# Optimization experiments

Hardware: AMD Instinct MI355X
Metric: run time of the kernel (lower is better)

Reference implementation:

```python
import jax, jax.numpy as jnp
import numpy as np

N = 4096
F_IN = 512
F_OUT = 64
H = 8
ALPHA = 0.2
NEG_BIG = -9e15


def setup_inputs() -> dict:
    key = jax.random.key(0)
    ks = jax.random.split(key, 7)
    h = jax.random.normal(ks[0], (N, F_IN), dtype=jnp.float32)
    mask = jax.random.randint(ks[1], (N, N), 0, 2, dtype=jnp.int32)
    # per-head linear W: weight [H, F_IN, F_OUT], bias [H, F_OUT] (xavier-ish scale)
    w_scale = 1.414 * np.sqrt(6.0 / (F_IN + F_OUT))
    W = jax.random.uniform(ks[2], (H, F_IN, F_OUT), dtype=jnp.float32, minval=-w_scale, maxval=w_scale)
    bW = jnp.zeros((H, F_OUT), dtype=jnp.float32)
    # attention linear A: [2*F_OUT, 1] split into a_l (acts on Wh_i) and a_r (acts on Wh_j)
    a_scale = 1.414 * np.sqrt(6.0 / (2 * F_OUT + 1))
    a_l = jax.random.uniform(ks[3], (H, F_OUT), dtype=jnp.float32, minval=-a_scale, maxval=a_scale)
    a_r = jax.random.uniform(ks[4], (H, F_OUT), dtype=jnp.float32, minval=-a_scale, maxval=a_scale)
    bA = jnp.zeros((H,), dtype=jnp.float32)
    return {"h": h, "mask": mask, "W": W, "bW": bW, "a_l": a_l, "a_r": a_r, "bA": bA}


def reference(h, mask, W, bW, a_l, a_r, bA):
    # Wh: [H, N, F_OUT]
    Wh = jnp.einsum('ni,hio->hno', h, W) + bW[:, None, :]
    # A([Wh_i ; Wh_j]) decomposed as outer sum: e[h,i,j] = a_l.Wh_i + a_r.Wh_j + bA
    el = jnp.einsum('hno,ho->hn', Wh, a_l)  # [H, N]
    er = jnp.einsum('hno,ho->hn', Wh, a_r)  # [H, N]
    e = el[:, :, None] + er[:, None, :] + bA[:, None, None]  # [H, N, N]
    e = jax.nn.leaky_relu(e, negative_slope=ALPHA)
    e = jnp.where(mask[None] > 0, e, NEG_BIG)
    a = jax.nn.softmax(e, axis=-1)  # softmax over neighbors j (dim=1 in torch)
    # dropout omitted (eval mode / deterministic reference)
    aWh = jnp.einsum('hij,hjo->hio', a, Wh)  # [H, N, F_OUT]
    out = jax.nn.elu(aWh)  # last=False
    # concat heads along feature dim -> [N, H*F_OUT]
    return jnp.transpose(out, (1, 0, 2)).reshape(N, H * F_OUT)
```

## Files before the change

### kernel.cpp

```cpp
#include <hip/hip_runtime.h>
#include <hip/hip_bf16.h>

#define NN 4096
#define FIN 512
#define FOUT 64
#define NH 8
#define ALPHA 0.2f

typedef unsigned int uint;
typedef unsigned short ushort;
typedef unsigned char uchar;
typedef unsigned long long ull;
typedef __attribute__((ext_vector_type(8))) short short8;
typedef __attribute__((ext_vector_type(4))) float floatx4;

__device__ __forceinline__ float bf2f(ushort s) { return __uint_as_float(((uint)s) << 16); }
__device__ __forceinline__ ushort f2bf(float f) {
    uint u = __float_as_uint(f);
    u += 0x7fffu + ((u >> 16) & 1u);
    return (ushort)(u >> 16);
}

__device__ __forceinline__ int detect_bf16(const ushort* __restrict__ hraw) {
    int lane = threadIdx.x & 63;
    float a = fabsf(bf2f(hraw[2 * lane]));
    ull bal = __ballot(a >= 1e-3f && a <= 100.0f);
    return __popcll(bal) >= 32;
}

#define PM_BLKS 8192
#define CV_BLKS 1024
#define TW_BLKS 32

__global__ __launch_bounds__(256) void prep_kernel(
    const int* __restrict__ mask, uchar* __restrict__ mb,
    const void* __restrict__ hraw, ushort* __restrict__ bh,
    const void* __restrict__ Wraw, ushort* __restrict__ WT)
{
    const int b = blockIdx.x, t = threadIdx.x;
    if (b < PM_BLKS) {
        size_t gid = (size_t)b * 256 + t;
        const int* p = mask + gid * 8;
        int4 aa = *(const int4*)p;
        int4 bb = *(const int4*)(p + 4);
        uint by = (uint)(aa.x > 0)        | ((uint)(aa.y > 0) << 1)
                | ((uint)(aa.z > 0) << 2) | ((uint)(aa.w > 0) << 3)
                | ((uint)(bb.x > 0) << 4) | ((uint)(bb.y > 0) << 5)
                | ((uint)(bb.z > 0) << 6) | ((uint)(bb.w > 0) << 7);
        mb[gid] = (uchar)by;
    } else if (b < PM_BLKS + CV_BLKS) {
        int isbf = detect_bf16((const ushort*)hraw);
        size_t e0 = ((size_t)(b - PM_BLKS) * 256 + t) * 8;
        if (isbf) {
            *(uint4*)(bh + e0) = *(const uint4*)((const ushort*)hraw + e0);
        } else {
            const float* s = (const float*)hraw + e0;
            float4 f0 = *(const float4*)s;
            float4 f1 = *(const float4*)(s + 4);
            uint4 o;
            o.x = (uint)f2bf(f0.x) | ((uint)f2bf(f0.y) << 16);
            o.y = (uint)f2bf(f0.z) | ((uint)f2bf(f0.w) << 16);
            o.z = (uint)f2bf(f1.x) | ((uint)f2bf(f1.y) << 16);
            o.w = (uint)f2bf(f1.z) | ((uint)f2bf(f1.w) << 16);
            *(uint4*)(bh + e0) = o;
        }
    } else {
        int isbf = detect_bf16((const ushort*)hraw);
        int b2 = b - PM_BLKS - CV_BLKS;
        int h = b2 >> 2, kq = b2 & 3;
        int o = t & 63, sub = t >> 6;
        int kbase = kq * 128 + sub * 32;
        uint pk[16];
#pragma unroll
        for (int kk = 0; kk < 32; kk += 2) {
            float v0, v1;
            size_t s0 = ((size_t)h * FIN + kbase + kk) * FOUT + o;
            size_t s1 = s0 + FOUT;
            if (isbf) { v0 = bf2f(((const ushort*)Wraw)[s0]); v1 = bf2f(((const ushort*)Wraw)[s1]); }
            else      { v0 = ((const float*)Wraw)[s0];        v1 = ((const float*)Wraw)[s1]; }
            pk[kk >> 1] = (uint)f2bf(v0) | ((uint)f2bf(v1) << 16);
        }
        ushort* dst = WT + ((size_t)h * FOUT + o) * FIN + kbase;
#pragma unroll
        for (int q = 0; q < 4; q++)
            *(uint4*)(dst + q * 8) = make_uint4(pk[q*4], pk[q*4+1], pk[q*4+2], pk[q*4+3]);
    }
}

__global__ __launch_bounds__(256) void khv_kernel(const float* __restrict__ er,
                                                  float* __restrict__ Kh,
                                                  float* __restrict__ vt,
                                                  float* __restrict__ zt) {
    __shared__ float red[256];
    int h = blockIdx.x >> 3, sl = blockIdx.x & 7, t = threadIdx.x;
    float m = -3.0e38f;
    for (int j = t; j < NN; j += 256) m = fmaxf(m, er[(size_t)h * NN + j]);
    red[t] = m;
    __syncthreads();
    for (int s = 128; s >= 1; s >>= 1) {
        if (t < s) red[t] = fmaxf(red[t], red[t + s]);
        __syncthreads();
    }
    float kh = red[0];
    if (t == 0 && sl == 0) Kh[h] = kh;
    int j = sl * 512 + t;
#pragma unroll
    for (int q = 0; q < 2; q++, j += 256) {
        float d = er[(size_t)h * NN + j] - kh;
        vt[(size_t)h * NN + j] = __expf(d);
        zt[(size_t)h * NN + j] = __expf(ALPHA * d);
    }
}

__global__ __launch_bounds__(256) void wh_kernel(
    const ushort* __restrict__ hmat, const ushort* __restrict__ WT,
    const void* __restrict__ bWr, const void* __restrict__ alr,
    const void* __restrict__ arr, const void* __restrict__ bAr,
    const ushort* __restrict__ hraw,
    ushort* __restrict__ WhT, float* __restrict__ el, float* __restrict__ er)
{
    __shared__ __align__(16) ushort sT[64][72];
    const int t = threadIdx.x, lane = t & 63, wid = t >> 6;
    const int head = blockIdx.y, rbase = blockIdx.x * 64;
    const int lm = lane & 15, lq = lane >> 4;

    floatx4 C[4];
#pragma unroll
    for (int cg = 0; cg < 4; cg++) C[cg] = (floatx4){0.f, 0.f, 0.f, 0.f};

    const ushort* Ap = hmat + (size_t)(rbase + wid * 16 + lm) * FIN + lq * 8;
    const ushort* Bp = WT + (size_t)head * FOUT * FIN + (size_t)lm * FIN + lq * 8;

#pragma unroll
    for (int kc = 0; kc < 16; kc++) {
        short8 a = *(const short8*)(Ap + kc * 32);
#pragma unroll
        for (int cg = 0; cg < 4; cg++) {
            short8 b = *(const short8*)(Bp + (size_t)cg * 16 * FIN + kc * 32);
            C[cg] = __builtin_amdgcn_mfma_f32_16x16x32_bf16(a, b, C[cg], 0, 0, 0);
        }
    }

    const int isbf = detect_bf16(hraw);
    float bA = isbf ? bf2f(((const ushort*)bAr)[head]) : ((const float*)bAr)[head];
    float pel[4] = {0.f, 0.f, 0.f, 0.f}, per[4] = {0.f, 0.f, 0.f, 0.f};
#pragma unroll
    for (int cg = 0; cg < 4; cg++) {
        int o = head * FOUT + cg * 16 + lm;
        float bw = isbf ? bf2f(((const ushort*)bWr)[o]) : ((const float*)bWr)[o];
        float av = isbf ? bf2f(((const ushort*)alr)[o]) : ((const float*)alr)[o];
        float rv = isbf ? bf2f(((const ushort*)arr)[o]) : ((const float*)arr)[o];
        ushort pk[4];
#pragma unroll
        for (int r = 0; r < 4; r++) {
            float v = C[cg][r] + bw;
            pel[r] += v * av;
            per[r] += v * rv;
            pk[r] = f2bf(v);
        }
        ushort4 p4; p4.x = pk[0]; p4.y = pk[1]; p4.z = pk[2]; p4.w = pk[3];
        *(ushort4*)(&sT[cg * 16 + lm][wid * 16 + lq * 4]) = p4;
    }
#pragma unroll
    for (int off = 1; off < 16; off <<= 1) {
#pragma unroll
        for (int r = 0; r < 4; r++) {
            pel[r] += __shfl_xor(pel[r], off);
            per[r] += __shfl_xor(per[r], off);
        }
    }
    if (lm == 0) {
#pragma unroll
        for (int r = 0; r < 4; r++) {
            int row = rbase + wid * 16 + lq * 4 + r;
            el[(size_t)head * NN + row] = pel[r];
            er[(size_t)head * NN + row] = per[r] + bA;
        }
    }
    __syncthreads();
    {
        int o = t >> 2, ch = t & 3;
        uint4 v0 = *(const uint4*)(&sT[o][ch * 16]);
        uint4 v1 = *(const uint4*)(&sT[o][ch * 16 + 8]);
        ushort* d = WhT + ((size_t)head * FOUT + o) * NN + rbase + ch * 16;
        *(uint4*)d = v0;
        *(uint4*)(d + 8) = v1;
    }
}

__device__ __forceinline__ uint ppair(float v0, float v1, float z0, float z1,
                                      uint m2, float ui, float wi) {
    float p0 = fmaxf(ui * v0, wi * z0);
    float p1 = fmaxf(ui * v1, wi * z1);
    uint k0 = (uint)0 - (m2 & 1u);
    uint k1 = (uint)0 - ((m2 >> 1) & 1u);
    p0 = __uint_as_float(__float_as_uint(p0) & k0);
    p1 = __uint_as_float(__float_as_uint(p1) & k1);
    __hip_bfloat162 r = __float22bfloat162_rn(make_float2(p0, p1));
    return *(uint*)&r;
}

__device__ __forceinline__ short8 pgen8(float4 va, float4 vb, float4 za, float4 zb,
                                        uint mby, float ui, float wi) {
    union { uint4 u; short8 s; } c;
    c.u.x = ppair(va.x, va.y, za.x, za.y, mby,      ui, wi);
    c.u.y = ppair(va.z, va.w, za.z, za.w, mby >> 2, ui, wi);
    c.u.z = ppair(vb.x, vb.y, zb.x, zb.y, mby >> 4, ui, wi);
    c.u.w = ppair(vb.z, vb.w, zb.z, zb.w, mby >> 6, ui, wi);
    return c.s;
}

#define VZLOAD(S, j0) do {                                      \
    v##S##a = *(const float4*)(gvt + (j0) + sh8);               \
    v##S##b = *(const float4*)(gvt + (j0) + sh8 + 4);           \
    v##S##c = *(const float4*)(gvt + (j0) + 32 + sh8);          \
    v##S##d = *(const float4*)(gvt + (j0) + 32 + sh8 + 4);      \
    z##S##a = *(const float4*)(gzt + (j0) + sh8);               \
    z##S##b = *(const float4*)(gzt + (j0) + sh8 + 4);           \
    z##S##c = *(const float4*)(gzt + (j0) + 32 + sh8);          \
    z##S##d = *(const float4*)(gzt + (j0) + 32 + sh8 + 4);      \
} while (0)

__global__ __launch_bounds__(128, 1) void attn_kernel(
    const uchar* __restrict__ mb,
    const ushort* __restrict__ WhT,
    const float* __restrict__ el, const float* __restrict__ Kh,
    const float* __restrict__ vt, const float* __restrict__ zt,
    const ushort* __restrict__ hraw,
    void* __restrict__ outv)
{
    __shared__ __align__(16) ushort sB[2][64 * 72];

    const int t = threadIdx.x, lane = t & 63, wid = t >> 6;
    const int b = blockIdx.x;
    const int head = b & 7;
    const int ibase = (b >> 3) * 64;
    const int lm = lane & 15, lq = lane >> 4;
    const int sh8 = lq * 8;

    const float kh = Kh[head];
    const int rowa = ibase + wid * 32 + lm;
    const float xa = el[(size_t)head * NN + rowa] + kh;
    const float xb = el[(size_t)head * NN + rowa + 16] + kh;
    const float Ma = fmaxf(xa, ALPHA * xa);
    const float Mb = fmaxf(xb, ALPHA * xb);
    const float uia = __expf(xa - Ma), wia = __expf(ALPHA * xa - Ma);
    const float uib = __expf(xb - Mb), wib = __expf(ALPHA * xb - Mb);

    const int so = t >> 1;
    const int sc = (t & 1) * 32;
    const ushort* gB = WhT + ((size_t)head * FOUT + so) * NN + sc;
    const float* gvt = vt + (size_t)head * NN;
    const float* gzt = zt + (size_t)head * NN;
    const uchar* mra = mb + (size_t)rowa * 512;
    const uchar* mrb = mra + 16 * 512;

    uint4 rr0, rr1, rr2, rr3;
    uint2 mka_s, mkb_s;

    auto gload = [&](int j0) {
        rr0 = *(const uint4*)(gB + j0);
        rr1 = *(const uint4*)(gB + j0 + 8);
        rr2 = *(const uint4*)(gB + j0 + 16);
        rr3 = *(const uint4*)(gB + j0 + 24);
        mka_s = *(const uint2*)(mra + (j0 >> 3));
        mkb_s = *(const uint2*)(mrb + (j0 >> 3));
    };
    auto lwrite = [&](int buf) {
        ushort* d = &sB[buf][so * 72 + sc];
        *(uint4*)(d)      = rr0;
        *(uint4*)(d + 8)  = rr1;
        *(uint4*)(d + 16) = rr2;
        *(uint4*)(d + 24) = rr3;
    };

    float4 v0a, v0b, v0c, v0d, z0a, z0b, z0c, z0d;
    float4 v1a, v1b, v1c, v1d, z1a, z1b, z1c, z1d;

    const short8 ones = {0x3F80, 0x3F80, 0x3F80, 0x3F80, 0x3F80, 0x3F80, 0x3F80, 0x3F80};
    floatx4 Z = {0.f, 0.f, 0.f, 0.f};
    floatx4 C0 = Z, C1 = Z, C2 = Z, C3 = Z, Cd0 = Z;
    floatx4 C4 = Z, C5 = Z, C6 = Z, C7 = Z, Cd1 = Z;

    auto compute = [&](int buf, uint2 mka, uint2 mkb,
                       float4 va, float4 vb, float4 vc, float4 vd,
                       float4 za, float4 zb, float4 zc, float4 zd) {
        uint m0a = (mka.x >> sh8) & 0xFFu;
        uint m1a = (mka.y >> sh8) & 0xFFu;
        uint m0b = (mkb.x >> sh8) & 0xFFu;
        uint m1b = (mkb.y >> sh8) & 0xFFu;
        short8 a0 = pgen8(va, vb, za, zb, m0a, uia, wia);
        short8 a1 = pgen8(vc, vd, zc, zd, m1a, uia, wia);
        short8 a2 = pgen8(va, vb, za, zb, m0b, uib, wib);
        short8 a3 = pgen8(vc, vd, zc, zd, m1b, uib, wib);
        const ushort* base = &sB[buf][0];
        short8 b00 = *(const short8*)(base + (0  + lm) * 72 + sh8);
        short8 b10 = *(const short8*)(base + (16 + lm) * 72 + sh8);
        short8 b20 = *(const short8*)(base + (32 + lm) * 72 + sh8);
        short8 b30 = *(const short8*)(base + (48 + lm) * 72 + sh8);
        Cd0 = __builtin_amdgcn_mfma_f32_16x16x32_bf16(a0, ones, Cd0, 0, 0, 0);
        Cd1 = __builtin_amdgcn_mfma_f32_16x16x32_bf16(a2, ones, Cd1, 0, 0, 0);
        C0 = __builtin_amdgcn_mfma_f32_16x16x32_bf16(a0, b00, C0, 0, 0, 0);
        C4 = __builtin_amdgcn_mfma_f32_16x16x32_bf16(a2, b00, C4, 0, 0, 0);
        C1 = __builtin_amdgcn_mfma_f32_16x16x32_bf16(a0, b10, C1, 0, 0, 0);
        C5 = __builtin_amdgcn_mfma_f32_16x16x32_bf16(a2, b10, C5, 0, 0, 0);
        C2 = __builtin_amdgcn_mfma_f32_16x16x32_bf16(a0, b20, C2, 0, 0, 0);
        C6 = __builtin_amdgcn_mfma_f32_16x16x32_bf16(a2, b20, C6, 0, 0, 0);
        C3 = __builtin_amdgcn_mfma_f32_16x16x32_bf16(a0, b30, C3, 0, 0, 0);
        C7 = __builtin_amdgcn_mfma_f32_16x16x32_bf16(a2, b30, C7, 0, 0, 0);
        short8 b01 = *(const short8*)(base + (0  + lm) * 72 + 32 + sh8);
        short8 b11 = *(const short8*)(base + (16 + lm) * 72 + 32 + sh8);
        short8 b21 = *(const short8*)(base + (32 + lm) * 72 + 32 + sh8);
        short8 b31 = *(const short8*)(base + (48 + lm) * 72 + 32 + sh8);
        Cd0 = __builtin_amdgcn_mfma_f32_16x16x32_bf16(a1, ones, Cd0, 0, 0, 0);
        Cd1 = __builtin_amdgcn_mfma_f32_16x16x32_bf16(a3, ones, Cd1, 0, 0, 0);
        C0 = __builtin_amdgcn_mfma_f32_16x16x32_bf16(a1, b01, C0, 0, 0, 0);
        C4 = __builtin_amdgcn_mfma_f32_16x16x32_bf16(a3, b01, C4, 0, 0, 0);
        C1 = __builtin_amdgcn_mfma_f32_16x16x32_bf16(a1, b11, C1, 0, 0, 0);
        C5 = __builtin_amdgcn_mfma_f32_16x16x32_bf16(a3, b11, C5, 0, 0, 0);
        C2 = __builtin_amdgcn_mfma_f32_16x16x32_bf16(a1, b21, C2, 0, 0, 0);
        C6 = __builtin_amdgcn_mfma_f32_16x16x32_bf16(a3, b21, C6, 0, 0, 0);
        C3 = __builtin_amdgcn_mfma_f32_16x16x32_bf16(a1, b31, C3, 0, 0, 0);
        C7 = __builtin_amdgcn_mfma_f32_16x16x32_bf16(a3, b31, C7, 0, 0, 0);
    };

    uint2 mka0, mkb0, mka1, mkb1;
    gload(0);
    lwrite(0);
    mka0 = mka_s; mkb0 = mkb_s;
    gload(64);
    VZLOAD(0, 0);
    __syncthreads();

    for (int it = 0; it < 64; it += 2) {
        lwrite(1);
        mka1 = mka_s; mkb1 = mkb_s;
        gload(((it + 2) & 63) * 64);
        VZLOAD(1, (it + 1) * 64);
        compute(0, mka0, mkb0, v0a, v0b, v0c, v0d, z0a, z0b, z0c, z0d);
        __syncthreads();
        lwrite(0);
        mka0 = mka_s; mkb0 = mkb_s;
        gload(((it + 3) & 63) * 64);
        VZLOAD(0, ((it + 2) & 63) * 64);
        compute(1, mka1, mkb1, v1a, v1b, v1c, v1d, z1a, z1b, z1c, z1d);
        __syncthreads();
    }

    const int isbf = detect_bf16(hraw);
#pragma unroll
    for (int r = 0; r < 4; r++) {
        int ra = ibase + wid * 32 + lq * 4 + r;
        int rb = ra + 16;
        float inva = 1.f / Cd0[r];
        float invb = 1.f / Cd1[r];
        float x0 = C0[r] * inva; x0 = (x0 > 0.f) ? x0 : __expf(x0) - 1.f;
        float x1 = C1[r] * inva; x1 = (x1 > 0.f) ? x1 : __expf(x1) - 1.f;
        float x2 = C2[r] * inva; x2 = (x2 > 0.f) ? x2 : __expf(x2) - 1.f;
        float x3 = C3[r] * inva; x3 = (x3 > 0.f) ? x3 : __expf(x3) - 1.f;
        float y0 = C4[r] * invb; y0 = (y0 > 0.f) ? y0 : __expf(y0) - 1.f;
        float y1 = C5[r] * invb; y1 = (y1 > 0.f) ? y1 : __expf(y1) - 1.f;
        float y2 = C6[r] * invb; y2 = (y2 > 0.f) ? y2 : __expf(y2) - 1.f;
        float y3 = C7[r] * invb; y3 = (y3 > 0.f) ? y3 : __expf(y3) - 1.f;
        size_t basea = (size_t)ra * (NH * FOUT) + head * FOUT + lm;
        size_t baseb = (size_t)rb * (NH * FOUT) + head * FOUT + lm;
        if (isbf) {
            ushort* o = (ushort*)outv;
            o[basea + 0]  = f2bf(x0);
            o[basea + 16] = f2bf(x1);
            o[basea + 32] = f2bf(x2);
            o[basea + 48] = f2bf(x3);
            o[baseb + 0]  = f2bf(y0);
            o[baseb + 16] = f2bf(y1);
            o[baseb + 32] = f2bf(y2);
            o[baseb + 48] = f2bf(y3);
        } else {
            float* o = (float*)outv;
            o[basea + 0]  = x0;
            o[basea + 16] = x1;
            o[basea + 32] = x2;
            o[basea + 48] = x3;
            o[baseb + 0]  = y0;
            o[baseb + 16] = y1;
            o[baseb + 32] = y2;
            o[baseb + 48] = y3;
        }
    }
}

extern "C" void kernel_launch(void* const* d_in, const int* in_sizes, int n_in,
                              void* d_out, int out_size, void* d_ws, size_t ws_size,
                              hipStream_t stream)
{
    const void* hraw = d_in[0];
    const int*  mask = (const int*)d_in[1];
    const void* Wraw = d_in[2];
    const void* bWr  = d_in[3];
    const void* alr  = d_in[4];
    const void* arr  = d_in[5];
    const void* bAr  = d_in[6];

    char* w = (char*)d_ws;
    ushort* bh   = (ushort*)w;                  w += (size_t)NN * FIN * 2;
    ushort* WT   = (ushort*)w;                  w += (size_t)NH * FOUT * FIN * 2;
    ushort* WhT  = (ushort*)w;                  w += (size_t)NH * FOUT * NN * 2;
    float*  el   = (float*)w;                   w += (size_t)NH * NN * 4;
    float*  er   = (float*)w;                   w += (size_t)NH * NN * 4;
    float*  Kh   = (float*)w;                   w += 64;
    float*  vt   = (float*)w;                   w += (size_t)NH * NN * 4;
    float*  zt   = (float*)w;                   w += (size_t)NH * NN * 4;
    uchar*  mb   = (uchar*)w;                   w += (size_t)NN * 512;

    prep_kernel<<<PM_BLKS + CV_BLKS + TW_BLKS, 256, 0, stream>>>(
        mask, mb, hraw, bh, Wraw, WT);
    wh_kernel<<<dim3(NN / 64, NH), 256, 0, stream>>>(bh, WT, bWr, alr, arr, bAr,
                                                     (const ushort*)hraw, WhT, el, er);
    khv_kernel<<<64, 256, 0, stream>>>(er, Kh, vt, zt);
    attn_kernel<<<NN / 64 * NH, 128, 0, stream>>>(mb, WhT, el, Kh, vt, zt,
                                                  (const ushort*)hraw, d_out);
}
```

Baseline: 205.0 us.

## Split attention over neighbor dimension across waves with LDS reduction

Restructures the attention kernel so each block handles 32 rows with 4 waves, each wave covering a quarter of the neighbor columns, and merges partial accumulators through shared memory before the epilogue. The shared-memory double-buffered WhT staging and barriers in the main loop are dropped; waves now load B fragments straight from global memory. This doubles the block count and raises occupancy to get more parallelism and latency hiding, at the cost of more global/L2 traffic for WhT, which is re-read per row block with no LDS reuse, plus an extra reduction step.

```diff
diff --git a/kernel.cpp b/kernel.cpp
--- a/kernel.cpp
+++ b/kernel.cpp
@@ -210,18 +210,7 @@
     return c.s;
 }
 
-#define VZLOAD(S, j0) do {                                      \
-    v##S##a = *(const float4*)(gvt + (j0) + sh8);               \
-    v##S##b = *(const float4*)(gvt + (j0) + sh8 + 4);           \
-    v##S##c = *(const float4*)(gvt + (j0) + 32 + sh8);          \
-    v##S##d = *(const float4*)(gvt + (j0) + 32 + sh8 + 4);      \
-    z##S##a = *(const float4*)(gzt + (j0) + sh8);               \
-    z##S##b = *(const float4*)(gzt + (j0) + sh8 + 4);           \
-    z##S##c = *(const float4*)(gzt + (j0) + 32 + sh8);          \
-    z##S##d = *(const float4*)(gzt + (j0) + 32 + sh8 + 4);      \
-} while (0)
-
-__global__ __launch_bounds__(128, 1) void attn_kernel(
+__global__ __launch_bounds__(256, 4) void attn_kernel(
     const uchar* __restrict__ mb,
     const ushort* __restrict__ WhT,
     const float* __restrict__ el, const float* __restrict__ Kh,
@@ -229,17 +218,17 @@
     const ushort* __restrict__ hraw,
     void* __restrict__ outv)
 {
-    __shared__ __align__(16) ushort sB[2][64 * 72];
-
-    const int t = threadIdx.x, lane = t & 63, wid = t >> 6;
+    __shared__ __align__(16) float mg[3][64 * 44];
+
+    const int t = threadIdx.x, lane = t & 63, jq = t >> 6;
     const int b = blockIdx.x;
     const int head = b & 7;
-    const int ibase = (b >> 3) * 64;
+    const int ibase = (b >> 3) * 32;
     const int lm = lane & 15, lq = lane >> 4;
     const int sh8 = lq * 8;
 
     const float kh = Kh[head];
-    const int rowa = ibase + wid * 32 + lm;
+    const int rowa = ibase + lm;
     const float xa = el[(size_t)head * NN + rowa] + kh;
     const float xb = el[(size_t)head * NN + rowa + 16] + kh;
     const float Ma = fmaxf(xa, ALPHA * xa);
@@ -247,57 +236,39 @@
     const float uia = __expf(xa - Ma), wia = __expf(ALPHA * xa - Ma);
     const float uib = __expf(xb - Mb), wib = __expf(ALPHA * xb - Mb);
 
-    const int so = t >> 1;
-    const int sc = (t & 1) * 32;
-    const ushort* gB = WhT + ((size_t)head * FOUT + so) * NN + sc;
-    const float* gvt = vt + (size_t)head * NN;
-    const float* gzt = zt + (size_t)head * NN;
-    const uchar* mra = mb + (size_t)rowa * 512;
+    const int jbase = jq * 1024;
+    const ushort* gB = WhT + (size_t)head * FOUT * NN;
+    const float* gvt = vt + (size_t)head * NN + jbase;
+    const float* gzt = zt + (size_t)head * NN + jbase;
+    const uchar* mra = mb + (size_t)rowa * 512 + (jbase >> 3);
     const uchar* mrb = mra + 16 * 512;
-
-    uint4 rr0, rr1, rr2, rr3;
-    uint2 mka_s, mkb_s;
-
-    auto gload = [&](int j0) {
-        rr0 = *(const uint4*)(gB + j0);
-        rr1 = *(const uint4*)(gB + j0 + 8);
-        rr2 = *(const uint4*)(gB + j0 + 16);
-        rr3 = *(const uint4*)(gB + j0 + 24);
-        mka_s = *(const uint2*)(mra + (j0 >> 3));
-        mkb_s = *(const uint2*)(mrb + (j0 >> 3));
-    };
-    auto lwrite = [&](int buf) {
-        ushort* d = &sB[buf][so * 72 + sc];
-        *(uint4*)(d)      = rr0;
-        *(uint4*)(d + 8)  = rr1;
-        *(uint4*)(d + 16) = rr2;
-        *(uint4*)(d + 24) = rr3;
-    };
-
-    float4 v0a, v0b, v0c, v0d, z0a, z0b, z0c, z0d;
-    float4 v1a, v1b, v1c, v1d, z1a, z1b, z1c, z1d;
 
     const short8 ones = {0x3F80, 0x3F80, 0x3F80, 0x3F80, 0x3F80, 0x3F80, 0x3F80, 0x3F80};
     floatx4 Z = {0.f, 0.f, 0.f, 0.f};
     floatx4 C0 = Z, C1 = Z, C2 = Z, C3 = Z, Cd0 = Z;
     floatx4 C4 = Z, C5 = Z, C6 = Z, C7 = Z, Cd1 = Z;
 
-    auto compute = [&](int buf, uint2 mka, uint2 mkb,
-                       float4 va, float4 vb, float4 vc, float4 vd,
-                       float4 za, float4 zb, float4 zc, float4 zd) {
+#pragma unroll 2
+    for (int tile = 0; tile < 16; ++tile) {
+        const int j0 = jbase + tile * 64;
+        const int jl = tile * 64;
+        uint2 mka = *(const uint2*)(mra + tile * 8);
+        uint2 mkb = *(const uint2*)(mrb + tile * 8);
         uint m0a = (mka.x >> sh8) & 0xFFu;
         uint m1a = (mka.y >> sh8) & 0xFFu;
         uint m0b = (mkb.x >> sh8) & 0xFFu;
         uint m1b = (mkb.y >> sh8) & 0xFFu;
+
+        float4 va = *(const float4*)(gvt + jl + sh8);
+        float4 vb = *(const float4*)(gvt + jl + sh8 + 4);
+        float4 za = *(const float4*)(gzt + jl + sh8);
+        float4 zb = *(const float4*)(gzt + jl + sh8 + 4);
+        short8 b00 = *(const short8*)(gB + (size_t)(0  + lm) * NN + j0 + sh8);
+        short8 b10 = *(const short8*)(gB + (size_t)(16 + lm) * NN + j0 + sh8);
+        short8 b20 = *(const short8*)(gB + (size_t)(32 + lm) * NN + j0 + sh8);
+        short8 b30 = *(const short8*)(gB + (size_t)(48 + lm) * NN + j0 + sh8);
         short8 a0 = pgen8(va, vb, za, zb, m0a, uia, wia);
-        short8 a1 = pgen8(vc, vd, zc, zd, m1a, uia, wia);
         short8 a2 = pgen8(va, vb, za, zb, m0b, uib, wib);
-        short8 a3 = pgen8(vc, vd, zc, zd, m1b, uib, wib);
-        const ushort* base = &sB[buf][0];
-        short8 b00 = *(const short8*)(base + (0  + lm) * 72 + sh8);
-        short8 b10 = *(const short8*)(base + (16 + lm) * 72 + sh8);
-        short8 b20 = *(const short8*)(base + (32 + lm) * 72 + sh8);
-        short8 b30 = *(const short8*)(base + (48 + lm) * 72 + sh8);
         Cd0 = __builtin_amdgcn_mfma_f32_16x16x32_bf16(a0, ones, Cd0, 0, 0, 0);
         Cd1 = __builtin_amdgcn_mfma_f32_16x16x32_bf16(a2, ones, Cd1, 0, 0, 0);
         C0 = __builtin_amdgcn_mfma_f32_16x16x32_bf16(a0, b00, C0, 0, 0, 0);
@@ -308,10 +279,17 @@
         C6 = __builtin_amdgcn_mfma_f32_16x16x32_bf16(a2, b20, C6, 0, 0, 0);
         C3 = __builtin_amdgcn_mfma_f32_16x16x32_bf16(a0, b30, C3, 0, 0, 0);
         C7 = __builtin_amdgcn_mfma_f32_16x16x32_bf16(a2, b30, C7, 0, 0, 0);
-        short8 b01 = *(const short8*)(base + (0  + lm) * 72 + 32 + sh8);
-        short8 b11 = *(const short8*)(base + (16 + lm) * 72 + 32 + sh8);
-        short8 b21 = *(const short8*)(base + (32 + lm) * 72 + 32 + sh8);
-        short8 b31 = *(const short8*)(base + (48 + lm) * 72 + 32 + sh8);
+
+        float4 vc = *(const float4*)(gvt + jl + 32 + sh8);
+        float4 vd = *(const float4*)(gvt + jl + 32 + sh8 + 4);
+        float4 zc = *(const float4*)(gzt + jl + 32 + sh8);
+        float4 zd = *(const float4*)(gzt + jl + 32 + sh8 + 4);
+        short8 b01 = *(const short8*)(gB + (size_t)(0  + lm) * NN + j0 + 32 + sh8);
+        short8 b11 = *(const short8*)(gB + (size_t)(16 + lm) * NN + j0 + 32 + sh8);
+        short8 b21 = *(const short8*)(gB + (size_t)(32 + lm) * NN + j0 + 32 + sh8);
+        short8 b31 = *(const short8*)(gB + (size_t)(48 + lm) * NN + j0 + 32 + sh8);
+        short8 a1 = pgen8(vc, vd, zc, zd, m1a, uia, wia);
+        short8 a3 = pgen8(vc, vd, zc, zd, m1b, uib, wib);
         Cd0 = __builtin_amdgcn_mfma_f32_16x16x32_bf16(a1, ones, Cd0, 0, 0, 0);
         Cd1 = __builtin_amdgcn_mfma_f32_16x16x32_bf16(a3, ones, Cd1, 0, 0, 0);
         C0 = __builtin_amdgcn_mfma_f32_16x16x32_bf16(a1, b01, C0, 0, 0, 0);
@@ -322,68 +300,65 @@
         C6 = __builtin_amdgcn_mfma_f32_16x16x32_bf16(a3, b21, C6, 0, 0, 0);
         C3 = __builtin_amdgcn_mfma_f32_16x16x32_bf16(a1, b31, C3, 0, 0, 0);
         C7 = __builtin_amdgcn_mfma_f32_16x16x32_bf16(a3, b31, C7, 0, 0, 0);
-    };
-
-    uint2 mka0, mkb0, mka1, mkb1;
-    gload(0);
-    lwrite(0);
-    mka0 = mka_s; mkb0 = mkb_s;
-    gload(64);
-    VZLOAD(0, 0);
+    }
+
+    if (jq > 0) {
+        float* p = &mg[jq - 1][lane * 44];
+        *(floatx4*)(p + 0)  = C0;  *(floatx4*)(p + 4)  = C1;
+        *(floatx4*)(p + 8)  = C2;  *(floatx4*)(p + 12) = C3;
+        *(floatx4*)(p + 16) = C4;  *(floatx4*)(p + 20) = C5;
+        *(floatx4*)(p + 24) = C6;  *(floatx4*)(p + 28) = C7;
+        *(floatx4*)(p + 32) = Cd0; *(floatx4*)(p + 36) = Cd1;
+    }
     __syncthreads();
-
-    for (int it = 0; it < 64; it += 2) {
-        lwrite(1);
-        mka1 = mka_s; mkb1 = mkb_s;
-        gload(((it + 2) & 63) * 64);
-        VZLOAD(1, (it + 1) * 64);
-        compute(0, mka0, mkb0, v0a, v0b, v0c, v0d, z0a, z0b, z0c, z0d);
-        __syncthreads();
-        lwrite(0);
-        mka0 = mka_s; mkb0 = mkb_s;
-        gload(((it + 3) & 63) * 64);
-        VZLOAD(0, ((it + 2) & 63) * 64);
-        compute(1, mka1, mkb1, v1a, v1b, v1c, v1d, z1a, z1b, z1c, z1d);
-        __syncthreads();
-    }
-
-    const int isbf = detect_bf16(hraw);
-#pragma unroll
-    for (int r = 0; r < 4; r++) {
-        int ra = ibase + wid * 32 + lq * 4 + r;
-        int rb = ra + 16;
-        float inva = 1.f / Cd0[r];
-        float invb = 1.f / Cd1[r];
-        float x0 = C0[r] * inva; x0 = (x0 > 0.f) ? x0 : __expf(x0) - 1.f;
-        float x1 = C1[r] * inva; x1 = (x1 > 0.f) ? x1 : __expf(x1) - 1.f;
-        float x2 = C2[r] * inva; x2 = (x2 > 0.f) ? x2 : __expf(x2) - 1.f;
-        float x3 = C3[r] * inva; x3 = (x3 > 0.f) ? x3 : __expf(x3) - 1.f;
-        float y0 = C4[r] * invb; y0 = (y0 > 0.f) ? y0 : __expf(y0) - 1.f;
-        float y1 = C5[r] * invb; y1 = (y1 > 0.f) ? y1 : __expf(y1) - 1.f;
-        float y2 = C6[r] * invb; y2 = (y2 > 0.f) ? y2 : __expf(y2) - 1.f;
-        float y3 = C7[r] * invb; y3 = (y3 > 0.f) ? y3 : __expf(y3) - 1.f;
-        size_t basea = (size_t)ra * (NH * FOUT) + head * FOUT + lm;
-        size_t baseb = (size_t)rb * (NH * FOUT) + head * FOUT + lm;
-        if (isbf) {
-            ushort* o = (ushort*)outv;
-            o[basea + 0]  = f2bf(x0);
-            o[basea + 16] = f2bf(x1);
-            o[basea + 32] = f2bf(x2);
-            o[basea + 48] = f2bf(x3);
-            o[baseb + 0]  = f2bf(y0);
-            o[baseb + 16] = f2bf(y1);
-            o[baseb + 32] = f2bf(y2);
-            o[baseb + 48] = f2bf(y3);
-        } else {
-            float* o = (float*)outv;
-            o[basea + 0]  = x0;
-            o[basea + 16] = x1;
-            o[basea + 32] = x2;
-            o[basea + 48] = x3;
-            o[baseb + 0]  = y0;
-            o[baseb + 16] = y1;
-            o[baseb + 32] = y2;
-            o[baseb + 48] = y3;
+    if (jq == 0) {
+#pragma unroll
+        for (int s = 0; s < 3; s++) {
+            const float* p = &mg[s][lane * 44];
+            C0 += *(const floatx4*)(p + 0);   C1 += *(const floatx4*)(p + 4);
+            C2 += *(const floatx4*)(p + 8);   C3 += *(const floatx4*)(p + 12);
+            C4 += *(const floatx4*)(p + 16);  C5 += *(const floatx4*)(p + 20);
+            C6 += *(const floatx4*)(p + 24);  C7 += *(const floatx4*)(p + 28);
+            Cd0 += *(const floatx4*)(p + 32); Cd1 += *(const floatx4*)(p + 36);
+        }
+        const int isbf = detect_bf16(hraw);
+#pragma unroll
+        for (int r = 0; r < 4; r++) {
+            int ra = ibase + lq * 4 + r;
+            int rb = ra + 16;
+            float inva = 1.f / Cd0[r];
+            float invb = 1.f / Cd1[r];
+            float x0 = C0[r] * inva; x0 = (x0 > 0.f) ? x0 : __expf(x0) - 1.f;
+            float x1 = C1[r] * inva; x1 = (x1 > 0.f) ? x1 : __expf(x1) - 1.f;
+            float x2 = C2[r] * inva; x2 = (x2 > 0.f) ? x2 : __expf(x2) - 1.f;
+            float x3 = C3[r] * inva; x3 = (x3 > 0.f) ? x3 : __expf(x3) - 1.f;
+            float y0 = C4[r] * invb; y0 = (y0 > 0.f) ? y0 : __expf(y0) - 1.f;
+            float y1 = C5[r] * invb; y1 = (y1 > 0.f) ? y1 : __expf(y1) - 1.f;
+            float y2 = C6[r] * invb; y2 = (y2 > 0.f) ? y2 : __expf(y2) - 1.f;
+            float y3 = C7[r] * invb; y3 = (y3 > 0.f) ? y3 : __expf(y3) - 1.f;
+            size_t basea = (size_t)ra * (NH * FOUT) + head * FOUT + lm;
+            size_t baseb = (size_t)rb * (NH * FOUT) + head * FOUT + lm;
+            if (isbf) {
+                ushort* o = (ushort*)outv;
+                o[basea + 0]  = f2bf(x0);
+                o[basea + 16] = f2bf(x1);
+                o[basea + 32] = f2bf(x2);
+                o[basea + 48] = f2bf(x3);
+                o[baseb + 0]  = f2bf(y0);
+                o[baseb + 16] = f2bf(y1);
+                o[baseb + 32] = f2bf(y2);
+                o[baseb + 48] = f2bf(y3);
+            } else {
+                float* o = (float*)outv;
+                o[basea + 0]  = x0;
+                o[basea + 16] = x1;
+                o[basea + 32] = x2;
+                o[basea + 48] = x3;
+                o[baseb + 0]  = y0;
+                o[baseb + 16] = y1;
+                o[baseb + 32] = y2;
+                o[baseb + 48] = y3;
+            }
         }
     }
 }
@@ -416,6 +391,6 @@
     wh_kernel<<<dim3(NN / 64, NH), 256, 0, stream>>>(bh, WT, bWr, alr, arr, bAr,
                                                      (const ushort*)hraw, WhT, el, er);
     khv_kernel<<<64, 256, 0, stream>>>(er, Kh, vt, zt);
-    attn_kernel<<<NN / 64 * NH, 128, 0, stream>>>(mb, WhT, el, Kh, vt, zt,
-                                                  (const ushort*)hraw, d_out);
-}
+    attn_kernel<<<128 * NH, 256, 0, stream>>>(mb, WhT, el, Kh, vt, zt,
+                                              (const ushort*)hraw, d_out);
+}
```

Result: slower. 216.9 us (+5.8%).
